# Kernel optimization log

Hardware: AMD Instinct MI355X
Metric: run time of the kernel (lower is better)

## Reference

```python
import jax, jax.numpy as jnp
import numpy as np

N_NODES = 50000   # field_size == number of graph nodes
N_EDGES = 800000  # avg degree 16
VOCAB = 200000    # feature_size
EMB = 64          # embedding_size == in_dim
HID = 64          # num_hidden
SLOPE = 0.2       # leaky relu negative slope


def setup_inputs() -> dict:
    key = jax.random.key(0)
    ks = jax.random.split(key, 20)
    s = 0.05
    d = {}
    d["features"] = jax.random.randint(ks[0], (8, N_NODES), 0, VOCAB, dtype=jnp.int32)
    d["feature_values"] = jax.random.uniform(ks[1], (8, N_NODES), dtype=jnp.float32)
    d["src"] = jax.random.randint(ks[2], (N_EDGES,), 0, N_NODES, dtype=jnp.int32)
    d["dst"] = jax.random.randint(ks[3], (N_EDGES,), 0, N_NODES, dtype=jnp.int32)
    d["emb"] = jax.random.normal(ks[4], (VOCAB, EMB), jnp.float32) * s
    # layer 0: in=64 -> heads=2, out=64 (no residual)
    d["W0"]  = jax.random.normal(ks[5], (EMB, 2 * HID), jnp.float32) * s
    d["al0"] = jax.random.normal(ks[6], (2, HID), jnp.float32) * s
    d["ar0"] = jax.random.normal(ks[7], (2, HID), jnp.float32) * s
    d["b0"]  = jnp.zeros((2 * HID,), jnp.float32)
    # layer 1: in=128 -> heads=2, out=64 (identity residual since in == heads*out)
    d["W1"]  = jax.random.normal(ks[8], (2 * HID, 2 * HID), jnp.float32) * s
    d["al1"] = jax.random.normal(ks[9], (2, HID), jnp.float32) * s
    d["ar1"] = jax.random.normal(ks[10], (2, HID), jnp.float32) * s
    d["b1"]  = jnp.zeros((2 * HID,), jnp.float32)
    # output layer: in=128 -> heads=1, out=64 (projected residual), no activation
    d["W2"]    = jax.random.normal(ks[11], (2 * HID, EMB), jnp.float32) * s
    d["al2"]   = jax.random.normal(ks[12], (1, EMB), jnp.float32) * s
    d["ar2"]   = jax.random.normal(ks[13], (1, EMB), jnp.float32) * s
    d["b2"]    = jnp.zeros((EMB,), jnp.float32)
    d["resW2"] = jax.random.normal(ks[14], (2 * HID, EMB), jnp.float32) * s
    return d


def _gat_layer(h, src, dst, W, al, ar, b, res, act):
    """DGL-style GATConv. h: [N, in], W: [in, H*D], al/ar: [H, D]."""
    N = h.shape[0]
    H, D = al.shape
    fh = (h @ W).reshape(N, H, D)                      # [N, H, D]
    el = jnp.einsum('nhd,hd->nh', fh, al)              # [N, H]
    er = jnp.einsum('nhd,hd->nh', fh, ar)              # [N, H]
    e = jax.nn.leaky_relu(el[src] + er[dst], SLOPE)    # [E, H]
    # edge softmax grouped by destination node
    m = jax.ops.segment_max(e, dst, num_segments=N)
    m = jnp.where(jnp.isfinite(m), m, 0.0)
    ex = jnp.exp(e - m[dst])
    den = jax.ops.segment_sum(ex, dst, num_segments=N)
    alpha = ex / jnp.maximum(den[dst], 1e-9)           # [E, H]
    out = jax.ops.segment_sum(alpha[:, :, None] * fh[src], dst, num_segments=N)  # [N, H, D]
    if res is not None:
        out = out + res
    out = out + b.reshape(H, D)
    if act:
        out = jax.nn.elu(out)
    return out


def reference(features, feature_values, src, dst, emb,
              W0, al0, ar0, b0, W1, al1, ar1, b1,
              W2, al2, ar2, b2, resW2):
    # embedding lookup scaled by feature values: [B, field, emb]
    fe = emb[features] * feature_values[..., None]
    h = fe[0]                                          # [N_NODES, EMB]
    # layer 0: no residual, elu, flatten heads
    h = _gat_layer(h, src, dst, W0, al0, ar0, b0, None, True).reshape(N_NODES, -1)
    # layer 1: identity residual (in == heads*out), elu, flatten heads
    res1 = h.reshape(N_NODES, 2, HID)
    h = _gat_layer(h, src, dst, W1, al1, ar1, b1, res1, True).reshape(N_NODES, -1)
    # output layer: projected residual, no activation, mean over heads
    res2 = (h @ resW2).reshape(N_NODES, 1, EMB)
    logits = _gat_layer(h, src, dst, W2, al2, ar2, b2, res2, False).mean(axis=1)
    return logits
```

## Files before the change

### kernel.cpp

```cpp
#include <hip/hip_runtime.h>
#include <hip/hip_fp16.h>


typedef __attribute__((ext_vector_type(8))) short short8;
typedef __attribute__((ext_vector_type(4))) float float4v;

__device__ __forceinline__ float lrelu(float x){ return fmaxf(x, 0.2f*x); }

__device__ __forceinline__ unsigned short f2bf(float f){
  unsigned int u = __float_as_uint(f);
  u += 0x7fffu + ((u >> 16) & 1u);
  return (unsigned short)(u >> 16);
}
__device__ __forceinline__ unsigned short f2h(float f){
  return __half_as_ushort(__float2half(f));
}
__device__ __forceinline__ float2 h2f2(unsigned v){
  __half2 h = *reinterpret_cast<__half2*>(&v);
  return __half22float2(h);
}
__device__ __forceinline__ int bperm(int idx, int v){
  return __builtin_amdgcn_ds_bpermute(idx, v);
}
__device__ __forceinline__ float bperm_f(int idx, int v){
  return __int_as_float(__builtin_amdgcn_ds_bpermute(idx, v));
}

__global__ void k_zero_i32(int* __restrict__ p, int n){
  int i = blockIdx.x*blockDim.x + threadIdx.x;
  if (i < n) p[i] = 0;
}

__global__ void k_hist_rank(const int* __restrict__ dst, int* __restrict__ counts,
                            int* __restrict__ rank, int E){
  int i = blockIdx.x*blockDim.x + threadIdx.x;
  if (i < E){
    int d = dst[i];
    rank[i] = atomicAdd(&counts[d], 1);
  }
}

__global__ void k_scan_local(const int* __restrict__ counts, int* __restrict__ row_ptr,
                             int* __restrict__ bsum, int N){
  __shared__ int s[256];
  int t = threadIdx.x, g = blockIdx.x*256 + t;
  int v = (g < N) ? counts[g] : 0;
  s[t] = v; __syncthreads();
  #pragma unroll
  for (int off = 1; off < 256; off <<= 1){
    int x = 0;
    if (t >= off) x = s[t-off];
    __syncthreads();
    s[t] += x;
    __syncthreads();
  }
  if (g < N) row_ptr[g+1] = s[t];
  if (g == 0 && t == 0) row_ptr[0] = 0;
  if (t == 255) bsum[blockIdx.x] = s[255];
}

__global__ void k_scan_top(int* __restrict__ bsum, int nb){
  __shared__ int s[256];
  int t = threadIdx.x;
  int v = (t < nb) ? bsum[t] : 0;
  s[t] = v; __syncthreads();
  #pragma unroll
  for (int off = 1; off < 256; off <<= 1){
    int x = 0;
    if (t >= off) x = s[t-off];
    __syncthreads();
    s[t] += x;
    __syncthreads();
  }
  if (t < nb) bsum[t] = s[t] - v;
}

__global__ void k_scan_fix(int* __restrict__ row_ptr, const int* __restrict__ bsum, int N){
  int g = blockIdx.x*256 + threadIdx.x;
  if (g < N && blockIdx.x > 0) row_ptr[g+1] += bsum[blockIdx.x];
}

__global__ void k_scatter2(const int* __restrict__ src, const int* __restrict__ dst,
                           const int* __restrict__ rank, const int* __restrict__ row_ptr,
                           int* __restrict__ ssrc, int E){
  int i = blockIdx.x*blockDim.x + threadIdx.x;
  if (i < E) ssrc[row_ptr[dst[i]] + rank[i]] = src[i];
}

__global__ void k_wprep_all(const float* __restrict__ W0, const float* __restrict__ W1,
                            const float* __restrict__ W2, const float* __restrict__ rW2,
                            unsigned short* __restrict__ Wt0, unsigned short* __restrict__ Wt1,
                            unsigned short* __restrict__ Wt2){
  int id = blockIdx.x*256 + threadIdx.x;
  if (id < 128*64){
    int n = id/64, k = id%64;
    Wt0[n*64 + k] = f2bf(W0[k*128 + n]);
  } else if (id < 128*64 + 128*128){
    int i = id - 128*64; int n = i/128, k = i%128;
    Wt1[n*128 + k] = f2bf(W1[k*128 + n]);
  } else if (id < 128*64 + 2*128*128){
    int i = id - 128*64 - 128*128; int n = i/128, k = i%128;
    float v = (n < 64) ? W2[k*64 + n] : rW2[k*64 + (n - 64)];
    Wt2[n*128 + k] = f2bf(v);
  }
}

template<int IN, int H, bool EMBED>
__global__ __launch_bounds__(256) void k_gemm_mfma(
    const unsigned short* __restrict__ hb,
    const int* __restrict__ feat, const float* __restrict__ fv,
    const float* __restrict__ embp,
    const unsigned short* __restrict__ Wt,
    const float* __restrict__ al, const float* __restrict__ ar,
    unsigned short* __restrict__ fhb,
    float* __restrict__ elr, int N){
  constexpr int KS = IN/32;
  constexpr int LDP = IN + 8;
  __shared__ unsigned short Wt_s[128*LDP];
  const int t = threadIdx.x;
  const int lane = t & 63, wid = t >> 6;
  const int l15 = lane & 15, quad = lane >> 4;
  const int row0 = blockIdx.x*64 + wid*16;

  for (int id = t; id < 128*(IN/8); id += 256){
    int r = id/(IN/8), seg = id%(IN/8);
    ((uint4*)(Wt_s + r*LDP))[seg] = ((const uint4*)(Wt + (size_t)r*IN))[seg];
  }
  short8 a[KS];
  int arow = row0 + l15;
  if (EMBED){
    if (arow < N){
      const float* er2 = embp + (size_t)feat[arow]*64;
      float sc = fv[arow];
      #pragma unroll
      for (int s = 0; s < KS; s++){
        const float4* p = (const float4*)(er2 + s*32 + quad*8);
        float4 v0 = p[0], v1 = p[1];
        short8 ta;
        ta[0] = (short)f2bf(v0.x*sc); ta[1] = (short)f2bf(v0.y*sc);
        ta[2] = (short)f2bf(v0.z*sc); ta[3] = (short)f2bf(v0.w*sc);
        ta[4] = (short)f2bf(v1.x*sc); ta[5] = (short)f2bf(v1.y*sc);
        ta[6] = (short)f2bf(v1.z*sc); ta[7] = (short)f2bf(v1.w*sc);
        a[s] = ta;
      }
    } else {
      #pragma unroll
      for (int s = 0; s < KS; s++) a[s] = short8{0,0,0,0,0,0,0,0};
    }
  } else {
    #pragma unroll
    for (int s = 0; s < KS; s++){
      if (arow < N) a[s] = *(const short8*)(hb + (size_t)arow*IN + s*32 + quad*8);
      else          a[s] = short8{0,0,0,0,0,0,0,0};
    }
  }
  __syncthreads();

  float4v acc[8];
  #pragma unroll
  for (int nt = 0; nt < 8; nt++) acc[nt] = float4v{0.f,0.f,0.f,0.f};
  #pragma unroll
  for (int nt = 0; nt < 8; nt++){
    #pragma unroll
    for (int s = 0; s < KS; s++){
      short8 b = *(const short8*)(Wt_s + (nt*16 + l15)*LDP + s*32 + quad*8);
      acc[nt] = __builtin_amdgcn_mfma_f32_16x16x32_bf16(a[s], b, acc[nt], 0, 0, 0);
    }
  }

  float alc[8], arc[8];
  #pragma unroll
  for (int nt = 0; nt < 8; nt++){
    bool hv = (H == 2) || (nt < 4);
    alc[nt] = hv ? al[nt*16 + l15] : 0.f;
    arc[nt] = hv ? ar[nt*16 + l15] : 0.f;
  }
  #pragma unroll
  for (int reg = 0; reg < 4; reg++){
    int row = row0 + quad*4 + reg;
    bool rv = row < N;
    if (rv){
      #pragma unroll
      for (int nt = 0; nt < 8; nt++)
        fhb[(size_t)row*128 + nt*16 + l15] = f2h(acc[nt][reg]);
    }
    float pel0 = 0.f, per0 = 0.f, pel1 = 0.f, per1 = 0.f;
    #pragma unroll
    for (int nt = 0; nt < 4; nt++){
      pel0 += acc[nt][reg]*alc[nt];     per0 += acc[nt][reg]*arc[nt];
      pel1 += acc[nt+4][reg]*alc[nt+4]; per1 += acc[nt+4][reg]*arc[nt+4];
    }
    #pragma unroll
    for (int off = 1; off < 16; off <<= 1){
      pel0 += __shfl_xor(pel0, off, 64);
      pel1 += __shfl_xor(pel1, off, 64);
      per0 += __shfl_xor(per0, off, 64);
      per1 += __shfl_xor(per1, off, 64);
    }
    if (l15 == 0 && rv){
      elr[row*4+0] = pel0;
      elr[row*4+1] = (H == 2) ? pel1 : 0.f;
      elr[row*4+2] = per0;
      elr[row*4+3] = (H == 2) ? per1 : 0.f;
    }
  }
}

template<int H>
__global__ __launch_bounds__(256) void k_agg(
    const unsigned short* __restrict__ fhb,
    const float* __restrict__ elr,
    const int* __restrict__ row_ptr, const int* __restrict__ ssrc,
    const float* __restrict__ bias, const float* __restrict__ res,
    int act, int res_from_fh,
    float* __restrict__ out, int out_ld, unsigned* __restrict__ outb, int N){
  int lane = threadIdx.x & 63, wid = threadIdx.x >> 6;
  int n = blockIdx.x*4 + wid;
  if (n >= N) return;
  int beg = row_ptr[n], end = row_ptr[n+1];
  float er0 = elr[n*4+2];
  float er1 = (H == 2) ? elr[n*4+3] : 0.f;

  float x0 = 0.f, x1 = 0.f;
  int s_first = 0;
  {
    int i = beg + lane;
    if (i < end){
      s_first = ssrc[i];
      float2 el = *(const float2*)(elr + s_first*4);
      x0 = __expf(fminf(lrelu(el.x + er0), 30.f));
      if (H == 2) x1 = __expf(fminf(lrelu(el.y + er1), 30.f));
    }
  }
  float d0 = x0, d1 = x1;
  for (int i = beg + lane + 64; i < end; i += 64){
    int s = ssrc[i];
    float2 el = *(const float2*)(elr + s*4);
    d0 += __expf(fminf(lrelu(el.x + er0), 30.f));
    if (H == 2) d1 += __expf(fminf(lrelu(el.y + er1), 30.f));
  }
  #pragma unroll
  for (int off = 32; off >= 1; off >>= 1){
    d0 += __shfl_xor(d0, off, 64);
    if (H == 2) d1 += __shfl_xor(d1, off, 64);
  }
  float rd0 = d0 > 0.f ? 1.f/d0 : 0.f;
  float rd1 = (H == 2 && d1 > 0.f) ? 1.f/d1 : 0.f;

  const uint4* fh4 = (const uint4*)fhb;
  const int g = (H == 2) ? (lane >> 4) : (lane >> 3);
  const int c = (H == 2) ? (lane & 15) : (lane & 7);
  const int head32 = (H == 2 && c >= 8) ? 32 : 0;
  float acc[8];
  #pragma unroll
  for (int k = 0; k < 8; k++) acc[k] = 0.f;

  for (int base = beg; base < end; base += 64){
    int s = 0; float a0 = 0.f, a1 = 0.f;
    {
      int i = base + lane;
      if (i < end){
        if (base == beg){
          s = s_first;
          a0 = x0 * rd0; if (H == 2) a1 = x1 * rd1;
        } else {
          s = ssrc[i];
          float2 el = *(const float2*)(elr + s*4);
          a0 = __expf(fminf(lrelu(el.x + er0), 30.f)) * rd0;
          if (H == 2) a1 = __expf(fminf(lrelu(el.y + er1), 30.f)) * rd1;
        }
      }
    }
    int cnt = min(64, end - base);
    if (H == 2){
      float a1x = __shfl_xor(a1, 32, 64);
      float a0x = __shfl_xor(a0, 32, 64);
      int ap  = __float_as_int((lane < 32) ? a0  : a1x);
      int ap2 = __float_as_int((lane < 32) ? a0x : a1);
      for (int j0 = 0; j0 < cnt; j0 += 8){
        int apx = (j0 < 32) ? ap : ap2;
        int jb = j0 & 31;
        int sj[2]; uint4 w[2]; float aj[2];
        #pragma unroll
        for (int u = 0; u < 2; u++) sj[u] = bperm((j0 + 4*u + g) << 2, s);
        #pragma unroll
        for (int u = 0; u < 2; u++) w[u] = fh4[(size_t)(unsigned)sj[u]*16 + c];
        #pragma unroll
        for (int u = 0; u < 2; u++) aj[u] = bperm_f((head32 + jb + 4*u + g) << 2, apx);
        #pragma unroll
        for (int u = 0; u < 2; u++){
          const unsigned* wp = (const unsigned*)&w[u];
          #pragma unroll
          for (int q = 0; q < 4; q++){
            float2 f = h2f2(wp[q]);
            acc[2*q]   = fmaf(f.x, aj[u], acc[2*q]);
            acc[2*q+1] = fmaf(f.y, aj[u], acc[2*q+1]);
          }
        }
      }
    } else {
      int av = __float_as_int(a0);
      for (int j0 = 0; j0 < cnt; j0 += 8){
        int sj = bperm((j0 + g) << 2, s);
        uint4 w = fh4[(size_t)(unsigned)sj*16 + c];
        float aj = bperm_f((j0 + g) << 2, av);
        const unsigned* wp = (const unsigned*)&w;
        #pragma unroll
        for (int q = 0; q < 4; q++){
          float2 f = h2f2(wp[q]);
          acc[2*q]   = fmaf(f.x, aj, acc[2*q]);
          acc[2*q+1] = fmaf(f.y, aj, acc[2*q+1]);
        }
      }
    }
  }

  #pragma unroll
  for (int k = 0; k < 8; k++){
    if (H == 1) acc[k] += __shfl_xor(acc[k], 8, 64);
    acc[k] += __shfl_xor(acc[k], 16, 64);
    acc[k] += __shfl_xor(acc[k], 32, 64);
  }

  if (H == 2){
    if (lane < 16){
      int cc = lane;
      float o[8];
      const float4* b4 = (const float4*)bias;
      float4 ba = b4[cc*2], bb = b4[cc*2+1];
      o[0]=acc[0]+ba.x; o[1]=acc[1]+ba.y; o[2]=acc[2]+ba.z; o[3]=acc[3]+ba.w;
      o[4]=acc[4]+bb.x; o[5]=acc[5]+bb.y; o[6]=acc[6]+bb.z; o[7]=acc[7]+bb.w;
      if (res){
        const float4* r4 = (const float4*)(res + (size_t)n*128);
        float4 ra = r4[cc*2], rb = r4[cc*2+1];
        o[0]+=ra.x; o[1]+=ra.y; o[2]+=ra.z; o[3]+=ra.w;
        o[4]+=rb.x; o[5]+=rb.y; o[6]+=rb.z; o[7]+=rb.w;
      }
      if (act){
        #pragma unroll
        for (int k = 0; k < 8; k++) o[k] = o[k] > 0.f ? o[k] : expm1f(o[k]);
      }
      if (out){
        float4* o4 = (float4*)(out + (size_t)n*out_ld);
        o4[cc*2]   = make_float4(o[0], o[1], o[2], o[3]);
        o4[cc*2+1] = make_float4(o[4], o[5], o[6], o[7]);
      }
      if (outb){
        uint4 ob;
        ob.x = (unsigned)f2bf(o[0]) | ((unsigned)f2bf(o[1]) << 16);
        ob.y = (unsigned)f2bf(o[2]) | ((unsigned)f2bf(o[3]) << 16);
        ob.z = (unsigned)f2bf(o[4]) | ((unsigned)f2bf(o[5]) << 16);
        ob.w = (unsigned)f2bf(o[6]) | ((unsigned)f2bf(o[7]) << 16);
        *(uint4*)(outb + (size_t)n*64 + cc*4) = ob;
      }
    }
  } else {
    if (lane < 8){
      int cc = lane;
      float o[8];
      #pragma unroll
      for (int k = 0; k < 8; k++) o[k] = acc[k] + bias[cc*8 + k];
      if (res_from_fh){
        uint4 r = fh4[(size_t)n*16 + 8 + cc];
        const unsigned* rp = (const unsigned*)&r;
        #pragma unroll
        for (int q = 0; q < 4; q++){
          float2 f = h2f2(rp[q]);
          o[2*q] += f.x; o[2*q+1] += f.y;
        }
      }
      float4* o4 = (float4*)(out + (size_t)n*out_ld);
      o4[cc*2]   = make_float4(o[0], o[1], o[2], o[3]);
      o4[cc*2+1] = make_float4(o[4], o[5], o[6], o[7]);
    }
  }
}

extern "C" void kernel_launch(void* const* d_in, const int* in_sizes, int n_in,
                              void* d_out, int out_size, void* d_ws, size_t ws_size,
                              hipStream_t stream) {
  const int*   feat = (const int*)  d_in[0];
  const float* fv   = (const float*)d_in[1];
  const int*   src  = (const int*)  d_in[2];
  const int*   dst  = (const int*)  d_in[3];
  const float* emb  = (const float*)d_in[4];
  const float* W0   = (const float*)d_in[5];
  const float* al0  = (const float*)d_in[6];
  const float* ar0  = (const float*)d_in[7];
  const float* b0   = (const float*)d_in[8];
  const float* W1   = (const float*)d_in[9];
  const float* al1  = (const float*)d_in[10];
  const float* ar1  = (const float*)d_in[11];
  const float* b1   = (const float*)d_in[12];
  const float* W2   = (const float*)d_in[13];
  const float* al2  = (const float*)d_in[14];
  const float* ar2  = (const float*)d_in[15];
  const float* b2   = (const float*)d_in[16];
  const float* rW2  = (const float*)d_in[17];
  const int N = in_sizes[0] / 8;
  const int E = in_sizes[2];

  size_t off = 0;
  auto alloc = [&](size_t bytes) -> void* {
    void* p = (char*)d_ws + off;
    off = (off + bytes + 255) & ~(size_t)255;
    return p;
  };
  unsigned short* P1 = (unsigned short*)alloc((size_t)N*128*sizeof(unsigned short));
  float* P2     = (float*)alloc((size_t)N*128*sizeof(float));
  unsigned short* hb = (unsigned short*)alloc((size_t)N*128*sizeof(unsigned short));
  float* elr    = (float*)alloc((size_t)N*4*sizeof(float));
  int* row_ptr  = (int*)alloc((size_t)(N+1)*sizeof(int));
  int* counts   = (int*)alloc((size_t)N*sizeof(int));
  int* rank     = (int*)alloc((size_t)E*sizeof(int));
  int* ssrc     = (int*)alloc((size_t)E*sizeof(int));
  int* bsum     = (int*)alloc(256*sizeof(int));
  unsigned short* Wt0 = (unsigned short*)alloc((size_t)128*64*sizeof(unsigned short));
  unsigned short* Wt1 = (unsigned short*)alloc((size_t)128*128*sizeof(unsigned short));
  unsigned short* Wt2 = (unsigned short*)alloc((size_t)128*128*sizeof(unsigned short));

  int nb1 = (N + 255) / 256;
  k_zero_i32<<<(N + 255)/256, 256, 0, stream>>>(counts, N);
  k_hist_rank<<<(E + 255)/256, 256, 0, stream>>>(dst, counts, rank, E);
  k_scan_local<<<nb1, 256, 0, stream>>>(counts, row_ptr, bsum, N);
  k_scan_top<<<1, 256, 0, stream>>>(bsum, nb1);
  k_scan_fix<<<nb1, 256, 0, stream>>>(row_ptr, bsum, N);
  k_scatter2<<<(E + 255)/256, 256, 0, stream>>>(src, dst, rank, row_ptr, ssrc, E);
  k_wprep_all<<<(128*64 + 2*128*128 + 255)/256, 256, 0, stream>>>(
      W0, W1, W2, rW2, Wt0, Wt1, Wt2);

  int gt = (N + 63)/64;
  int nagg = (N + 3)/4;
  k_gemm_mfma<64,2,true><<<gt, 256, 0, stream>>>(nullptr, feat, fv, emb,
                                                 Wt0, al0, ar0, P1, elr, N);
  k_agg<2><<<nagg, 256, 0, stream>>>(P1, elr, row_ptr, ssrc, b0, nullptr,
                                     1, 0, P2, 128, (unsigned*)hb, N);
  k_gemm_mfma<128,2,false><<<gt, 256, 0, stream>>>(hb, nullptr, nullptr, nullptr,
                                                   Wt1, al1, ar1, P1, elr, N);
  k_agg<2><<<nagg, 256, 0, stream>>>(P1, elr, row_ptr, ssrc, b1, P2,
                                     1, 0, nullptr, 128, (unsigned*)hb, N);
  k_gemm_mfma<128,1,false><<<gt, 256, 0, stream>>>(hb, nullptr, nullptr, nullptr,
                                                   Wt2, al2, ar2, P1, elr, N);
  k_agg<1><<<nagg, 256, 0, stream>>>(P1, elr, row_ptr, ssrc, b2, nullptr,
                                     0, 1, (float*)d_out, 64, nullptr, N);
}
```

Before: 335.1 us.

## Fuse softmax denominator into aggregation pass with deferred normalization

The aggregation kernel now computes the softmax denominator in the same pass that accumulates weighted features, and applies the reciprocal once at the end rather than normalizing each edge weight. This removes the separate first pass over edges (an extra round of ssrc/elr gathers and exps for high-degree nodes). The H=2 inner loop also moves from 2-way unrolled 8-edge steps to single 4-edge steps with byte-offset addressing, and ELU now uses __expf-1 in place of expm1f, which may lose precision near zero.

After: 332.0 us. No clear change (-0.9%).

```diff
diff --git a/kernel.cpp b/kernel.cpp
--- a/kernel.cpp
+++ b/kernel.cpp
@@ -15,15 +15,14 @@
 __device__ __forceinline__ unsigned short f2h(float f){
   return __half_as_ushort(__float2half(f));
 }
-__device__ __forceinline__ float2 h2f2(unsigned v){
-  __half2 h = *reinterpret_cast<__half2*>(&v);
-  return __half22float2(h);
-}
 __device__ __forceinline__ int bperm(int idx, int v){
   return __builtin_amdgcn_ds_bpermute(idx, v);
 }
 __device__ __forceinline__ float bperm_f(int idx, int v){
   return __int_as_float(__builtin_amdgcn_ds_bpermute(idx, v));
+}
+__device__ __forceinline__ float elu1(float x){
+  return x > 0.f ? x : (__expf(x) - 1.f);
 }
 
 __global__ void k_zero_i32(int* __restrict__ p, int n){
@@ -221,99 +220,71 @@
   float er0 = elr[n*4+2];
   float er1 = (H == 2) ? elr[n*4+3] : 0.f;
 
-  float x0 = 0.f, x1 = 0.f;
-  int s_first = 0;
-  {
-    int i = beg + lane;
+  const char* fhbB = (const char*)fhb;
+  const int g  = (H == 2) ? (lane >> 4) : (lane >> 3);
+  const int c  = (H == 2) ? (lane & 15) : (lane & 7);
+  const unsigned cb = (unsigned)c << 4;
+  const int hb4 = (H == 2 && c >= 8) ? (32 << 2) : 0;
+  const int g4 = g << 2;
+
+  float acc[8];
+  #pragma unroll
+  for (int k = 0; k < 8; k++) acc[k] = 0.f;
+  float den0 = 0.f, den1 = 0.f;
+
+  for (int base = beg; base < end; base += 64){
+    int s = 0; float e0 = 0.f, e1 = 0.f;
+    int i = base + lane;
     if (i < end){
-      s_first = ssrc[i];
-      float2 el = *(const float2*)(elr + s_first*4);
-      x0 = __expf(fminf(lrelu(el.x + er0), 30.f));
-      if (H == 2) x1 = __expf(fminf(lrelu(el.y + er1), 30.f));
-    }
-  }
-  float d0 = x0, d1 = x1;
-  for (int i = beg + lane + 64; i < end; i += 64){
-    int s = ssrc[i];
-    float2 el = *(const float2*)(elr + s*4);
-    d0 += __expf(fminf(lrelu(el.x + er0), 30.f));
-    if (H == 2) d1 += __expf(fminf(lrelu(el.y + er1), 30.f));
-  }
-  #pragma unroll
-  for (int off = 32; off >= 1; off >>= 1){
-    d0 += __shfl_xor(d0, off, 64);
-    if (H == 2) d1 += __shfl_xor(d1, off, 64);
-  }
-  float rd0 = d0 > 0.f ? 1.f/d0 : 0.f;
-  float rd1 = (H == 2 && d1 > 0.f) ? 1.f/d1 : 0.f;
-
-  const uint4* fh4 = (const uint4*)fhb;
-  const int g = (H == 2) ? (lane >> 4) : (lane >> 3);
-  const int c = (H == 2) ? (lane & 15) : (lane & 7);
-  const int head32 = (H == 2 && c >= 8) ? 32 : 0;
-  float acc[8];
-  #pragma unroll
-  for (int k = 0; k < 8; k++) acc[k] = 0.f;
-
-  for (int base = beg; base < end; base += 64){
-    int s = 0; float a0 = 0.f, a1 = 0.f;
-    {
-      int i = base + lane;
-      if (i < end){
-        if (base == beg){
-          s = s_first;
-          a0 = x0 * rd0; if (H == 2) a1 = x1 * rd1;
-        } else {
-          s = ssrc[i];
-          float2 el = *(const float2*)(elr + s*4);
-          a0 = __expf(fminf(lrelu(el.x + er0), 30.f)) * rd0;
-          if (H == 2) a1 = __expf(fminf(lrelu(el.y + er1), 30.f)) * rd1;
-        }
-      }
+      s = ssrc[i];
+      float2 el = *(const float2*)(elr + s*4);
+      e0 = __expf(fminf(lrelu(el.x + er0), 30.f));
+      if (H == 2) e1 = __expf(fminf(lrelu(el.y + er1), 30.f));
+      den0 += e0; den1 += e1;
     }
     int cnt = min(64, end - base);
     if (H == 2){
-      float a1x = __shfl_xor(a1, 32, 64);
-      float a0x = __shfl_xor(a0, 32, 64);
-      int ap  = __float_as_int((lane < 32) ? a0  : a1x);
-      int ap2 = __float_as_int((lane < 32) ? a0x : a1);
-      for (int j0 = 0; j0 < cnt; j0 += 8){
+      float e1x = __shfl_xor(e1, 32, 64);
+      float e0x = __shfl_xor(e0, 32, 64);
+      int ap  = __float_as_int((lane < 32) ? e0  : e1x);
+      int ap2 = __float_as_int((lane < 32) ? e0x : e1);
+      for (int j0 = 0; j0 < cnt; j0 += 4){
         int apx = (j0 < 32) ? ap : ap2;
-        int jb = j0 & 31;
-        int sj[2]; uint4 w[2]; float aj[2];
-        #pragma unroll
-        for (int u = 0; u < 2; u++) sj[u] = bperm((j0 + 4*u + g) << 2, s);
-        #pragma unroll
-        for (int u = 0; u < 2; u++) w[u] = fh4[(size_t)(unsigned)sj[u]*16 + c];
-        #pragma unroll
-        for (int u = 0; u < 2; u++) aj[u] = bperm_f((head32 + jb + 4*u + g) << 2, apx);
-        #pragma unroll
-        for (int u = 0; u < 2; u++){
-          const unsigned* wp = (const unsigned*)&w[u];
-          #pragma unroll
-          for (int q = 0; q < 4; q++){
-            float2 f = h2f2(wp[q]);
-            acc[2*q]   = fmaf(f.x, aj[u], acc[2*q]);
-            acc[2*q+1] = fmaf(f.y, aj[u], acc[2*q+1]);
-          }
-        }
-      }
-    } else {
-      int av = __float_as_int(a0);
-      for (int j0 = 0; j0 < cnt; j0 += 8){
-        int sj = bperm((j0 + g) << 2, s);
-        uint4 w = fh4[(size_t)(unsigned)sj*16 + c];
-        float aj = bperm_f((j0 + g) << 2, av);
-        const unsigned* wp = (const unsigned*)&w;
+        int sj = bperm(((j0 + g) << 2), s);
+        unsigned off = ((unsigned)sj << 8) + cb;
+        uint4 w = *(const uint4*)(fhbB + off);
+        float aj = bperm_f((((j0 & 31) + g) << 2) + hb4, apx);
+        const __half2* hp = (const __half2*)&w;
         #pragma unroll
         for (int q = 0; q < 4; q++){
-          float2 f = h2f2(wp[q]);
-          acc[2*q]   = fmaf(f.x, aj, acc[2*q]);
-          acc[2*q+1] = fmaf(f.y, aj, acc[2*q+1]);
+          acc[2*q]   = fmaf((float)hp[q].x, aj, acc[2*q]);
+          acc[2*q+1] = fmaf((float)hp[q].y, aj, acc[2*q+1]);
         }
       }
-    }
-  }
+    } else {
+      int av = __float_as_int(e0);
+      for (int j0 = 0; j0 < cnt; j0 += 8){
+        int sj = bperm((j0 << 2) + g4, s);
+        unsigned off = ((unsigned)sj << 8) + cb;
+        uint4 w = *(const uint4*)(fhbB + off);
+        float aj = bperm_f((j0 << 2) + g4, av);
+        const __half2* hp = (const __half2*)&w;
+        #pragma unroll
+        for (int q = 0; q < 4; q++){
+          acc[2*q]   = fmaf((float)hp[q].x, aj, acc[2*q]);
+          acc[2*q+1] = fmaf((float)hp[q].y, aj, acc[2*q+1]);
+        }
+      }
+    }
+  }
+
+  #pragma unroll
+  for (int off = 32; off >= 1; off >>= 1){
+    den0 += __shfl_xor(den0, off, 64);
+    if (H == 2) den1 += __shfl_xor(den1, off, 64);
+  }
+  float rd0 = den0 > 0.f ? 1.f/den0 : 0.f;
+  float rd1 = (H == 2 && den1 > 0.f) ? 1.f/den1 : 0.f;
 
   #pragma unroll
   for (int k = 0; k < 8; k++){
@@ -325,11 +296,14 @@
   if (H == 2){
     if (lane < 16){
       int cc = lane;
+      float rs = (cc < 8) ? rd0 : rd1;
       float o[8];
       const float4* b4 = (const float4*)bias;
       float4 ba = b4[cc*2], bb = b4[cc*2+1];
-      o[0]=acc[0]+ba.x; o[1]=acc[1]+ba.y; o[2]=acc[2]+ba.z; o[3]=acc[3]+ba.w;
-      o[4]=acc[4]+bb.x; o[5]=acc[5]+bb.y; o[6]=acc[6]+bb.z; o[7]=acc[7]+bb.w;
+      o[0]=fmaf(acc[0],rs,ba.x); o[1]=fmaf(acc[1],rs,ba.y);
+      o[2]=fmaf(acc[2],rs,ba.z); o[3]=fmaf(acc[3],rs,ba.w);
+      o[4]=fmaf(acc[4],rs,bb.x); o[5]=fmaf(acc[5],rs,bb.y);
+      o[6]=fmaf(acc[6],rs,bb.z); o[7]=fmaf(acc[7],rs,bb.w);
       if (res){
         const float4* r4 = (const float4*)(res + (size_t)n*128);
         float4 ra = r4[cc*2], rb = r4[cc*2+1];
@@ -338,7 +312,7 @@
       }
       if (act){
         #pragma unroll
-        for (int k = 0; k < 8; k++) o[k] = o[k] > 0.f ? o[k] : expm1f(o[k]);
+        for (int k = 0; k < 8; k++) o[k] = elu1(o[k]);
       }
       if (out){
         float4* o4 = (float4*)(out + (size_t)n*out_ld);
@@ -359,14 +333,15 @@
       int cc = lane;
       float o[8];
       #pragma unroll
-      for (int k = 0; k < 8; k++) o[k] = acc[k] + bias[cc*8 + k];
+      for (int k = 0; k < 8; k++) o[k] = fmaf(acc[k], rd0, bias[cc*8 + k]);
       if (res_from_fh){
+        const uint4* fh4 = (const uint4*)fhb;
         uint4 r = fh4[(size_t)n*16 + 8 + cc];
-        const unsigned* rp = (const unsigned*)&r;
+        const __half2* rp = (const __half2*)&r;
         #pragma unroll
         for (int q = 0; q < 4; q++){
-          float2 f = h2f2(rp[q]);
-          o[2*q] += f.x; o[2*q+1] += f.y;
+          o[2*q]   += (float)rp[q].x;
+          o[2*q+1] += (float)rp[q].y;
         }
       }
       float4* o4 = (float4*)(out + (size_t)n*out_ld);
```
